# Kernel tuning notes

Hardware: AMD Instinct MI355X
Metric: run time of the kernel (lower is better)

Reference implementation:

```python
import jax, jax.numpy as jnp
import numpy as np

B, C, L = 4, 256, 2048
HEADS, DIM_HEAD = 8, 64
HIDDEN = HEADS * DIM_HEAD  # 512


def setup_inputs() -> dict:
    key = jax.random.key(0)
    k1, k2, k3, k4 = jax.random.split(key, 4)
    x = jax.random.normal(k1, (B, C, L), dtype=jnp.float32)
    # Conv1d kernel_size=1 weights, squeezed to [out_ch, in_ch]
    w_qkv = jax.random.normal(k2, (3 * HIDDEN, C), dtype=jnp.float32) * (1.0 / np.sqrt(C))
    w_out = jax.random.normal(k3, (C, HIDDEN), dtype=jnp.float32) * (1.0 / np.sqrt(HIDDEN))
    b_out = jax.random.normal(k4, (C,), dtype=jnp.float32) * 0.01
    return {"x": x, "w_qkv": w_qkv, "w_out": w_out, "b_out": b_out}


def reference(x, w_qkv, w_out, b_out):
    b, c, l = x.shape
    scale = DIM_HEAD ** (-0.5)
    # pointwise conv == channel matmul
    qkv = jnp.einsum('oc,bcl->bol', w_qkv, x)  # [b, 3*hidden, l]
    q, k, v = jnp.split(qkv, 3, axis=1)        # each [b, hidden, l]
    def to_heads(t):
        return t.reshape(b, HEADS, DIM_HEAD, l)  # b h d l
    q, k, v = to_heads(q), to_heads(k), to_heads(v)
    q = q * scale
    sim = jnp.einsum('bhdi,bhdj->bhij', q, k)   # [b,h,l,l]
    attn = jax.nn.softmax(sim, axis=-1)          # stable softmax (max-subtract inside)
    out = jnp.einsum('bhij,bhdj->bhid', attn, v)  # [b,h,l,d]
    out = out.transpose(0, 1, 3, 2).reshape(b, HIDDEN, l)  # b (h d) l
    return jnp.einsum('oc,bcl->bol', w_out, out) + b_out[None, :, None]
```

## Files before the change

### kernel.cpp

```cpp
#include <hip/hip_runtime.h>

typedef unsigned short u16;
typedef __bf16 bf16x8 __attribute__((ext_vector_type(8)));
typedef float f32x4 __attribute__((ext_vector_type(4)));

#define MFMA16(a, b, c) __builtin_amdgcn_mfma_f32_16x16x32_bf16((a), (b), (c), 0, 0, 0)

#define Bn 4
#define Cn 256
#define Ln 2048
#define Hn 8
#define Dn 64
#define HID 512

__device__ __forceinline__ u16 bf16_rne(float f) {
  unsigned u = __builtin_bit_cast(unsigned, f);
  u += 0x7FFFu + ((u >> 16) & 1u);
  return (u16)(u >> 16);
}

__device__ __forceinline__ unsigned pack2(float a, float b) {
  return (unsigned)bf16_rne(a) | ((unsigned)bf16_rne(b) << 16);
}

__device__ __forceinline__ float fast_exp2(float x) {
#if __has_builtin(__builtin_amdgcn_exp2f)
  return __builtin_amdgcn_exp2f(x);
#else
  return exp2f(x);
#endif
}

__device__ __forceinline__ float fast_rcp(float x) {
#if __has_builtin(__builtin_amdgcn_rcpf)
  return __builtin_amdgcn_rcpf(x);
#else
  return 1.0f / x;
#endif
}

__device__ __forceinline__ void async_load16(const u16* g, u16* l) {
  __builtin_amdgcn_global_load_lds(
      (const __attribute__((address_space(1))) void*)g,
      (__attribute__((address_space(3))) void*)l, 16, 0, 0);
}

__global__ __launch_bounds__(256) void prep_weights(const float* __restrict__ wqkv,
                                                    const float* __restrict__ wout,
                                                    u16* __restrict__ wq,
                                                    u16* __restrict__ wo) {
  int i = blockIdx.x * 256 + threadIdx.x;
  const float QSCALE = 0.125f * 1.44269504088896340736f;
  if (i < 3 * HID * Cn) {
    float v = wqkv[i];
    if (i < HID * Cn) v *= QSCALE;
    wq[i] = bf16_rne(v);
  } else {
    int j = i - 3 * HID * Cn;
    wo[j] = bf16_rne(wout[j]);
  }
}

__global__ __launch_bounds__(256) void transpose_x(const float* __restrict__ x,
                                                   u16* __restrict__ xT) {
  __shared__ u16 tile[64][72];
  const int b = blockIdx.z, ct = blockIdx.y, lt = blockIdx.x;
  const int t = threadIdx.x;
  const float* xp = x + ((size_t)b * Cn + ct * 64) * Ln + lt * 64;
  for (int pass = 0; pass < 4; ++pass) {
    int c = pass * 16 + (t >> 4);
    int l4 = (t & 15) * 4;
    float4 v = *(const float4*)(xp + (size_t)c * Ln + l4);
    tile[l4 + 0][c] = bf16_rne(v.x);
    tile[l4 + 1][c] = bf16_rne(v.y);
    tile[l4 + 2][c] = bf16_rne(v.z);
    tile[l4 + 3][c] = bf16_rne(v.w);
  }
  __syncthreads();
  u16* op = xT + ((size_t)b * Ln + lt * 64) * Cn + ct * 64;
  for (int pass = 0; pass < 2; ++pass) {
    int id = pass * 256 + t;
    int l = id >> 3, c8 = (id & 7) * 8;
    *(uint4*)(op + (size_t)l * Cn + c8) = *(const uint4*)&tile[l][c8];
  }
}

__global__ __launch_bounds__(256) void qkv_gemm(const u16* __restrict__ wq,
                                                const u16* __restrict__ xT,
                                                u16* __restrict__ qT,
                                                u16* __restrict__ kT,
                                                u16* __restrict__ vv) {
  __shared__ u16 As[4096];
  __shared__ u16 Bs[4096];
  const int t = threadIdx.x;
  const int nt = blockIdx.x, mt = blockIdx.y, b = blockIdx.z;
  const int m0 = mt * 64, n0 = nt * 64;
  const int w = t >> 6, lane = t & 63, q = lane >> 4, ln = lane & 15;

  const u16* Ag = wq + (size_t)m0 * Cn;
  const u16* Bg = xT + ((size_t)b * Ln + n0) * Cn;

  f32x4 zf = {0.f, 0.f, 0.f, 0.f};
  f32x4 acc[4];
  for (int i = 0; i < 4; ++i) acc[i] = zf;

  for (int kk = 0; kk < 4; ++kk) {
    int k0 = kk * 64;
    for (int k2 = 0; k2 < 2; ++k2) {
      int reg = k2 * 4 + w;
      int r = reg * 8 + (lane >> 3);
      int c = (lane & 7) ^ (r & 7);
      async_load16(Ag + (size_t)r * Cn + k0 + c * 8, &As[reg * 512]);
      async_load16(Bg + (size_t)r * Cn + k0 + c * 8, &Bs[reg * 512]);
    }
    __syncthreads();
    int ar = w * 16 + ln;
    bf16x8 a0 = *(const bf16x8*)&As[ar * 64 + ((q ^ (ln & 7)) * 8)];
    bf16x8 a1 = *(const bf16x8*)&As[ar * 64 + (((q + 4) ^ (ln & 7)) * 8)];
    for (int n2 = 0; n2 < 4; ++n2) {
      int br = n2 * 16 + ln;
      bf16x8 b0 = *(const bf16x8*)&Bs[br * 64 + ((q ^ (ln & 7)) * 8)];
      bf16x8 b1 = *(const bf16x8*)&Bs[br * 64 + (((q + 4) ^ (ln & 7)) * 8)];
      acc[n2] = MFMA16(a0, b0, acc[n2]);
      acc[n2] = MFMA16(a1, b1, acc[n2]);
    }
    __syncthreads();
  }

  if (mt < 16) {
    int od0 = w * 16 + q * 4;
    int cw = od0 >> 3, lo = od0 & 7;
    for (int n2 = 0; n2 < 4; ++n2) {
      int l = n2 * 16 + ln;
      uint2 pk;
      pk.x = pack2(acc[n2][0], acc[n2][1]);
      pk.y = pack2(acc[n2][2], acc[n2][3]);
      *(uint2*)&As[l * 64 + ((cw ^ (l & 7)) * 8) + lo] = pk;
    }
    __syncthreads();
    u16* dst = (mt < 8) ? qT + (((size_t)b * Hn + mt) * Ln + n0) * Dn
                        : kT + (((size_t)b * Hn + (mt - 8)) * Ln + n0) * Dn;
    for (int pass = 0; pass < 2; ++pass) {
      int id = pass * 256 + t;
      int l = id >> 3, c = id & 7;
      *(uint4*)(dst + (size_t)l * Dn + c * 8) =
          *(const uint4*)&As[l * 64 + ((c ^ (l & 7)) * 8)];
    }
  } else {
    for (int n2 = 0; n2 < 4; ++n2) {
      int l = n2 * 16 + ln;
      int cl = l >> 3, lo = l & 7;
      for (int r = 0; r < 4; ++r) {
        int od = w * 16 + q * 4 + r;
        As[od * 64 + ((cl ^ (od & 7)) * 8) + lo] = bf16_rne(acc[n2][r]);
      }
    }
    __syncthreads();
    u16* dst = vv + ((size_t)b * HID + (mt - 16) * 64) * Ln + n0;
    for (int pass = 0; pass < 2; ++pass) {
      int id = pass * 256 + t;
      int od = id >> 3, c = id & 7;
      *(uint4*)(dst + (size_t)od * Ln + c * 8) =
          *(const uint4*)&As[od * 64 + ((c ^ (od & 7)) * 8)];
    }
  }
}

__global__ __launch_bounds__(256) void attention(const u16* __restrict__ qT,
                                                 const u16* __restrict__ kT,
                                                 const u16* __restrict__ vv,
                                                 u16* __restrict__ attT) {
  __shared__ u16 Kt[4096];
  __shared__ u16 Vt[4096];
  __shared__ u16 Ps[8192];
  const int t = threadIdx.x;
  const int qb = blockIdx.x, bh = blockIdx.y;
  const int b = bh >> 3, h = bh & 7;
  const int w = t >> 6, lane = t & 63, q = lane >> 4, ln = lane & 15;
  const int i0 = qb * 128 + w * 32;

  bf16x8 qa00, qa01, qa10, qa11;
  {
    const u16* qrow0 = qT + (((size_t)bh) * Ln + i0 + ln) * Dn;
    const u16* qrow1 = qT + (((size_t)bh) * Ln + i0 + 16 + ln) * Dn;
    qa00 = *(const bf16x8*)(qrow0 + q * 8);
    qa01 = *(const bf16x8*)(qrow0 + 32 + q * 8);
    qa10 = *(const bf16x8*)(qrow1 + q * 8);
    qa11 = *(const bf16x8*)(qrow1 + 32 + q * 8);
  }

  const u16* ksrc0 = kT + ((size_t)bh) * Ln * Dn;
  const u16* vsrc0 = vv + ((size_t)b * HID + h * Dn) * Ln;

  bf16x8 ones;
  for (int i = 0; i < 8; ++i) ones[i] = (__bf16)1.0f;

  f32x4 zf = {0.f, 0.f, 0.f, 0.f};
  f32x4 o_acc[2][4], l_acc[2];
  for (int it = 0; it < 2; ++it) {
    l_acc[it] = zf;
    for (int d = 0; d < 4; ++d) o_acc[it][d] = zf;
  }
  u16* pw0 = Ps + w * 2048;

  const int pr0 = w * 8 + (lane >> 3), pr1 = (4 + w) * 8 + (lane >> 3);
  const int pc0 = (lane & 7) ^ (pr0 & 7), pc1 = (lane & 7) ^ (pr1 & 7);
  const u16* kadr0 = ksrc0 + (size_t)pr0 * Dn + pc0 * 8;
  const u16* kadr1 = ksrc0 + (size_t)pr1 * Dn + pc1 * 8;
  const u16* vadr0 = vsrc0 + (size_t)pr0 * Ln + pc0 * 8;
  const u16* vadr1 = vsrc0 + (size_t)pr1 * Ln + pc1 * 8;

#define LOADKV(jt, K0, K1, V0, V1)                              \
  {                                                             \
    int j0_ = (jt) * 64;                                        \
    K0 = *(const uint4*)(kadr0 + (size_t)j0_ * Dn);             \
    K1 = *(const uint4*)(kadr1 + (size_t)j0_ * Dn);             \
    V0 = *(const uint4*)(vadr0 + j0_);                          \
    V1 = *(const uint4*)(vadr1 + j0_);                          \
  }

#define STOREKV(K0, K1, V0, V1)                                 \
  {                                                             \
    *(uint4*)&Kt[w * 512 + lane * 8] = K0;                      \
    *(uint4*)&Kt[(4 + w) * 512 + lane * 8] = K1;                \
    *(uint4*)&Vt[w * 512 + lane * 8] = V0;                      \
    *(uint4*)&Vt[(4 + w) * 512 + lane * 8] = V1;                \
  }

#define COMPUTE()                                                              \
  {                                                                            \
    f32x4 sv[2][4];                                                            \
    for (int n2 = 0; n2 < 4; ++n2) {                                           \
      int jr = n2 * 16 + ln;                                                   \
      bf16x8 k0f = *(const bf16x8*)&Kt[jr * 64 + ((q ^ (ln & 7)) * 8)];        \
      bf16x8 k1f = *(const bf16x8*)&Kt[jr * 64 + (((q + 4) ^ (ln & 7)) * 8)];  \
      f32x4 s0 = zf, s1 = zf;                                                  \
      s0 = MFMA16(k0f, qa00, s0);                                              \
      s0 = MFMA16(k1f, qa01, s0);                                              \
      s1 = MFMA16(k0f, qa10, s1);                                              \
      s1 = MFMA16(k1f, qa11, s1);                                              \
      sv[0][n2] = s0;                                                          \
      sv[1][n2] = s1;                                                          \
    }                                                                          \
    for (int it = 0; it < 2; ++it) {                                           \
      u16* pw = pw0 + it * 1024;                                               \
      for (int n2 = 0; n2 < 4; ++n2) {                                         \
        uint2 pk;                                                              \
        pk.x = pack2(fast_exp2(sv[it][n2][0]), fast_exp2(sv[it][n2][1]));      \
        pk.y = pack2(fast_exp2(sv[it][n2][2]), fast_exp2(sv[it][n2][3]));      \
        int jw = n2 * 16 + q * 4;                                              \
        int c_ = jw >> 3, lo_ = jw & 7;                                        \
        *(uint2*)&pw[ln * 64 + ((c_ ^ (ln & 7)) * 8) + lo_] = pk;              \
      }                                                                        \
    }                                                                          \
    for (int it = 0; it < 2; ++it) {                                           \
      u16* pw = pw0 + it * 1024;                                               \
      bf16x8 pa0 = *(const bf16x8*)&pw[ln * 64 + ((q ^ (ln & 7)) * 8)];        \
      bf16x8 pa1 = *(const bf16x8*)&pw[ln * 64 + (((q + 4) ^ (ln & 7)) * 8)];  \
      l_acc[it] = MFMA16(pa0, ones, l_acc[it]);                                \
      l_acc[it] = MFMA16(pa1, ones, l_acc[it]);                                \
      for (int d2 = 0; d2 < 4; ++d2) {                                         \
        int dr = d2 * 16 + ln;                                                 \
        bf16x8 v0f = *(const bf16x8*)&Vt[dr * 64 + ((q ^ (ln & 7)) * 8)];      \
        bf16x8 v1f = *(const bf16x8*)&Vt[dr * 64 + (((q + 4) ^ (ln & 7)) * 8)];\
        o_acc[it][d2] = MFMA16(pa0, v0f, o_acc[it][d2]);                       \
        o_acc[it][d2] = MFMA16(pa1, v1f, o_acc[it][d2]);                       \
      }                                                                        \
    }                                                                          \
  }

  uint4 ka0, ka1, wa0, wa1, kb0, kb1, wb0, wb1;
  LOADKV(0, ka0, ka1, wa0, wa1);
  for (int jt = 0; jt < 32; jt += 2) {
    if (jt) __syncthreads();
    STOREKV(ka0, ka1, wa0, wa1);
    __syncthreads();
    LOADKV(jt + 1, kb0, kb1, wb0, wb1);
    COMPUTE();
    __syncthreads();
    STOREKV(kb0, kb1, wb0, wb1);
    __syncthreads();
    if (jt + 2 < 32) LOADKV(jt + 2, ka0, ka1, wa0, wa1);
    COMPUTE();
  }
#undef LOADKV
#undef STOREKV
#undef COMPUTE

  for (int it = 0; it < 2; ++it) {
    for (int r = 0; r < 4; ++r) {
      float rinv = fast_rcp(l_acc[it][r]);
      int i = i0 + it * 16 + q * 4 + r;
      size_t base = ((size_t)b * Ln + i) * HID + h * Dn;
      for (int d2 = 0; d2 < 4; ++d2)
        attT[base + d2 * 16 + ln] = bf16_rne(o_acc[it][d2][r] * rinv);
    }
  }
}

__global__ __launch_bounds__(256) void out_gemm(const u16* __restrict__ wo,
                                                const u16* __restrict__ attT,
                                                const float* __restrict__ bout,
                                                float* __restrict__ out) {
  __shared__ u16 As[4096];
  __shared__ u16 Bs[4096];
  const int t = threadIdx.x;
  const int nt = blockIdx.x, mt = blockIdx.y, b = blockIdx.z;
  const int m0 = mt * 64, n0 = nt * 64;
  const int w = t >> 6, lane = t & 63, q = lane >> 4, ln = lane & 15;

  const u16* Ag = wo + (size_t)m0 * HID;
  const u16* Bg = attT + ((size_t)b * Ln + n0) * HID;

  f32x4 zf = {0.f, 0.f, 0.f, 0.f};
  f32x4 acc[4];
  for (int i = 0; i < 4; ++i) acc[i] = zf;

  const int pr0 = w * 8 + (lane >> 3), pr1 = (4 + w) * 8 + (lane >> 3);
  const int pc0 = (lane & 7) ^ (pr0 & 7), pc1 = (lane & 7) ^ (pr1 & 7);
  const u16* Aad0 = Ag + (size_t)pr0 * HID + pc0 * 8;
  const u16* Aad1 = Ag + (size_t)pr1 * HID + pc1 * 8;
  const u16* Bad0 = Bg + (size_t)pr0 * HID + pc0 * 8;
  const u16* Bad1 = Bg + (size_t)pr1 * HID + pc1 * 8;

#define LOADAB(kk, A0, A1, B0, B1)               \
  {                                              \
    int k0_ = (kk) * 64;                         \
    A0 = *(const uint4*)(Aad0 + k0_);            \
    A1 = *(const uint4*)(Aad1 + k0_);            \
    B0 = *(const uint4*)(Bad0 + k0_);            \
    B1 = *(const uint4*)(Bad1 + k0_);            \
  }

#define STOREAB(A0, A1, B0, B1)                  \
  {                                              \
    *(uint4*)&As[w * 512 + lane * 8] = A0;       \
    *(uint4*)&As[(4 + w) * 512 + lane * 8] = A1; \
    *(uint4*)&Bs[w * 512 + lane * 8] = B0;       \
    *(uint4*)&Bs[(4 + w) * 512 + lane * 8] = B1; \
  }

#define COMPUTEC()                                                             \
  {                                                                            \
    int ar = w * 16 + ln;                                                      \
    bf16x8 a0 = *(const bf16x8*)&As[ar * 64 + ((q ^ (ln & 7)) * 8)];           \
    bf16x8 a1 = *(const bf16x8*)&As[ar * 64 + (((q + 4) ^ (ln & 7)) * 8)];     \
    for (int n2 = 0; n2 < 4; ++n2) {                                           \
      int br = n2 * 16 + ln;                                                   \
      bf16x8 b0 = *(const bf16x8*)&Bs[br * 64 + ((q ^ (ln & 7)) * 8)];         \
      bf16x8 b1 = *(const bf16x8*)&Bs[br * 64 + (((q + 4) ^ (ln & 7)) * 8)];   \
      acc[n2] = MFMA16(a0, b0, acc[n2]);                                       \
      acc[n2] = MFMA16(a1, b1, acc[n2]);                                       \
    }                                                                          \
  }

  uint4 aa0, aa1, ba0, ba1, ab0, ab1, bb0, bb1;
  LOADAB(0, aa0, aa1, ba0, ba1);
  for (int kk = 0; kk < 8; kk += 2) {
    if (kk) __syncthreads();
    STOREAB(aa0, aa1, ba0, ba1);
    __syncthreads();
    LOADAB(kk + 1, ab0, ab1, bb0, bb1);
    COMPUTEC();
    __syncthreads();
    STOREAB(ab0, ab1, bb0, bb1);
    __syncthreads();
    if (kk + 2 < 8) LOADAB(kk + 2, aa0, aa1, ba0, ba1);
    COMPUTEC();
  }
#undef LOADAB
#undef STOREAB
#undef COMPUTEC

  float bias[4];
  for (int r = 0; r < 4; ++r) bias[r] = bout[m0 + w * 16 + q * 4 + r];
  for (int n2 = 0; n2 < 4; ++n2) {
    int l = n0 + n2 * 16 + ln;
    for (int r = 0; r < 4; ++r) {
      int o = m0 + w * 16 + q * 4 + r;
      out[((size_t)b * Cn + o) * Ln + l] = acc[n2][r] + bias[r];
    }
  }
}

extern "C" void kernel_launch(void* const* d_in, const int* in_sizes, int n_in,
                              void* d_out, int out_size, void* d_ws, size_t ws_size,
                              hipStream_t stream) {
  const float* x = (const float*)d_in[0];
  const float* wqkv = (const float*)d_in[1];
  const float* wout = (const float*)d_in[2];
  const float* bout = (const float*)d_in[3];
  float* out = (float*)d_out;
  char* ws = (char*)d_ws;

  u16* wq_b = (u16*)(ws + 0);
  u16* wo_b = (u16*)(ws + 786432);
  u16* xT   = (u16*)(ws + 1048576);
  u16* qT   = (u16*)(ws + 5242880);
  u16* kT   = (u16*)(ws + 13631488);
  u16* vv   = (u16*)(ws + 22020096);
  u16* attT = (u16*)(ws + 30408704);

  prep_weights<<<2048, 256, 0, stream>>>(wqkv, wout, wq_b, wo_b);
  transpose_x<<<dim3(32, 4, 4), 256, 0, stream>>>(x, xT);
  qkv_gemm<<<dim3(32, 24, 4), 256, 0, stream>>>(wq_b, xT, qT, kT, vv);
  attention<<<dim3(16, 32), 256, 0, stream>>>(qT, kT, vv, attT);
  out_gemm<<<dim3(32, 4, 4), 256, 0, stream>>>(wo_b, attT, bout, out);
}
```

Baseline: 153.3 us.

## Switch attention to 32x32 MFMA, merge prep kernels, register-pipeline QKV GEMM

The attention kernel now uses 32x32x16 bf16 MFMA tiles. The row sum is accumulated in registers and combined with a lane shuffle, replacing the extra MFMA against a ones vector, and a cheaper round-to-nearest pack is used for P. The weight-prep and x-transpose kernels are merged into one launch to save a launch. The QKV GEMM replaces async global-to-LDS loads with a register double-buffered load/store pipeline. The main targets are MFMA instruction count and softmax overhead in the attention inner loop, at the cost of more registers per thread and a new output lane mapping.

```diff
diff --git a/kernel.cpp b/kernel.cpp
--- a/kernel.cpp
+++ b/kernel.cpp
@@ -1,10 +1,13 @@
 #include <hip/hip_runtime.h>
 
 typedef unsigned short u16;
+typedef unsigned int u32;
 typedef __bf16 bf16x8 __attribute__((ext_vector_type(8)));
 typedef float f32x4 __attribute__((ext_vector_type(4)));
+typedef float f32x16 __attribute__((ext_vector_type(16)));
 
 #define MFMA16(a, b, c) __builtin_amdgcn_mfma_f32_16x16x32_bf16((a), (b), (c), 0, 0, 0)
+#define MFMA32(a, b, c) __builtin_amdgcn_mfma_f32_32x32x16_bf16((a), (b), (c), 0, 0, 0)
 
 #define Bn 4
 #define Cn 256
@@ -14,13 +17,19 @@
 #define HID 512
 
 __device__ __forceinline__ u16 bf16_rne(float f) {
-  unsigned u = __builtin_bit_cast(unsigned, f);
+  u32 u = __builtin_bit_cast(u32, f);
   u += 0x7FFFu + ((u >> 16) & 1u);
   return (u16)(u >> 16);
 }
 
 __device__ __forceinline__ unsigned pack2(float a, float b) {
   return (unsigned)bf16_rne(a) | ((unsigned)bf16_rne(b) << 16);
+}
+
+__device__ __forceinline__ u32 pk_hi(float lo, float hi) {
+  u32 a = __builtin_bit_cast(u32, lo) + 0x8000u;
+  u32 b = __builtin_bit_cast(u32, hi) + 0x8000u;
+  return (b & 0xFFFF0000u) | (a >> 16);
 }
 
 __device__ __forceinline__ float fast_exp2(float x) {
@@ -39,42 +48,38 @@
 #endif
 }
 
-__device__ __forceinline__ void async_load16(const u16* g, u16* l) {
-  __builtin_amdgcn_global_load_lds(
-      (const __attribute__((address_space(1))) void*)g,
-      (__attribute__((address_space(3))) void*)l, 16, 0, 0);
-}
-
-__global__ __launch_bounds__(256) void prep_weights(const float* __restrict__ wqkv,
-                                                    const float* __restrict__ wout,
-                                                    u16* __restrict__ wq,
-                                                    u16* __restrict__ wo) {
-  int i = blockIdx.x * 256 + threadIdx.x;
-  const float QSCALE = 0.125f * 1.44269504088896340736f;
-  if (i < 3 * HID * Cn) {
-    float v = wqkv[i];
-    if (i < HID * Cn) v *= QSCALE;
-    wq[i] = bf16_rne(v);
-  } else {
-    int j = i - 3 * HID * Cn;
-    wo[j] = bf16_rne(wout[j]);
-  }
-}
-
-__global__ __launch_bounds__(256) void transpose_x(const float* __restrict__ x,
-                                                   u16* __restrict__ xT) {
+__global__ __launch_bounds__(256) void prep_all(const float* __restrict__ wqkv,
+                                                const float* __restrict__ wout,
+                                                const float* __restrict__ x,
+                                                u16* __restrict__ wq,
+                                                u16* __restrict__ wo,
+                                                u16* __restrict__ xT) {
+  const int t = threadIdx.x;
+  if (blockIdx.x < 2048) {
+    int i = blockIdx.x * 256 + t;
+    const float QSCALE = 0.125f * 1.44269504088896340736f;
+    if (i < 3 * HID * Cn) {
+      float v = wqkv[i];
+      if (i < HID * Cn) v *= QSCALE;
+      wq[i] = bf16_rne(v);
+    } else {
+      int j = i - 3 * HID * Cn;
+      wo[j] = bf16_rne(wout[j]);
+    }
+    return;
+  }
   __shared__ u16 tile[64][72];
-  const int b = blockIdx.z, ct = blockIdx.y, lt = blockIdx.x;
-  const int t = threadIdx.x;
+  int v = blockIdx.x - 2048;
+  const int lt = v & 31, ct = (v >> 5) & 3, b = v >> 7;
   const float* xp = x + ((size_t)b * Cn + ct * 64) * Ln + lt * 64;
   for (int pass = 0; pass < 4; ++pass) {
     int c = pass * 16 + (t >> 4);
     int l4 = (t & 15) * 4;
-    float4 v = *(const float4*)(xp + (size_t)c * Ln + l4);
-    tile[l4 + 0][c] = bf16_rne(v.x);
-    tile[l4 + 1][c] = bf16_rne(v.y);
-    tile[l4 + 2][c] = bf16_rne(v.z);
-    tile[l4 + 3][c] = bf16_rne(v.w);
+    float4 vf = *(const float4*)(xp + (size_t)c * Ln + l4);
+    tile[l4 + 0][c] = bf16_rne(vf.x);
+    tile[l4 + 1][c] = bf16_rne(vf.y);
+    tile[l4 + 2][c] = bf16_rne(vf.z);
+    tile[l4 + 3][c] = bf16_rne(vf.w);
   }
   __syncthreads();
   u16* op = xT + ((size_t)b * Ln + lt * 64) * Cn + ct * 64;
@@ -104,224 +109,12 @@
   f32x4 acc[4];
   for (int i = 0; i < 4; ++i) acc[i] = zf;
 
-  for (int kk = 0; kk < 4; ++kk) {
-    int k0 = kk * 64;
-    for (int k2 = 0; k2 < 2; ++k2) {
-      int reg = k2 * 4 + w;
-      int r = reg * 8 + (lane >> 3);
-      int c = (lane & 7) ^ (r & 7);
-      async_load16(Ag + (size_t)r * Cn + k0 + c * 8, &As[reg * 512]);
-      async_load16(Bg + (size_t)r * Cn + k0 + c * 8, &Bs[reg * 512]);
-    }
-    __syncthreads();
-    int ar = w * 16 + ln;
-    bf16x8 a0 = *(const bf16x8*)&As[ar * 64 + ((q ^ (ln & 7)) * 8)];
-    bf16x8 a1 = *(const bf16x8*)&As[ar * 64 + (((q + 4) ^ (ln & 7)) * 8)];
-    for (int n2 = 0; n2 < 4; ++n2) {
-      int br = n2 * 16 + ln;
-      bf16x8 b0 = *(const bf16x8*)&Bs[br * 64 + ((q ^ (ln & 7)) * 8)];
-      bf16x8 b1 = *(const bf16x8*)&Bs[br * 64 + (((q + 4) ^ (ln & 7)) * 8)];
-      acc[n2] = MFMA16(a0, b0, acc[n2]);
-      acc[n2] = MFMA16(a1, b1, acc[n2]);
-    }
-    __syncthreads();
-  }
-
-  if (mt < 16) {
-    int od0 = w * 16 + q * 4;
-    int cw = od0 >> 3, lo = od0 & 7;
-    for (int n2 = 0; n2 < 4; ++n2) {
-      int l = n2 * 16 + ln;
-      uint2 pk;
-      pk.x = pack2(acc[n2][0], acc[n2][1]);
-      pk.y = pack2(acc[n2][2], acc[n2][3]);
-      *(uint2*)&As[l * 64 + ((cw ^ (l & 7)) * 8) + lo] = pk;
-    }
-    __syncthreads();
-    u16* dst = (mt < 8) ? qT + (((size_t)b * Hn + mt) * Ln + n0) * Dn
-                        : kT + (((size_t)b * Hn + (mt - 8)) * Ln + n0) * Dn;
-    for (int pass = 0; pass < 2; ++pass) {
-      int id = pass * 256 + t;
-      int l = id >> 3, c = id & 7;
-      *(uint4*)(dst + (size_t)l * Dn + c * 8) =
-          *(const uint4*)&As[l * 64 + ((c ^ (l & 7)) * 8)];
-    }
-  } else {
-    for (int n2 = 0; n2 < 4; ++n2) {
-      int l = n2 * 16 + ln;
-      int cl = l >> 3, lo = l & 7;
-      for (int r = 0; r < 4; ++r) {
-        int od = w * 16 + q * 4 + r;
-        As[od * 64 + ((cl ^ (od & 7)) * 8) + lo] = bf16_rne(acc[n2][r]);
-      }
-    }
-    __syncthreads();
-    u16* dst = vv + ((size_t)b * HID + (mt - 16) * 64) * Ln + n0;
-    for (int pass = 0; pass < 2; ++pass) {
-      int id = pass * 256 + t;
-      int od = id >> 3, c = id & 7;
-      *(uint4*)(dst + (size_t)od * Ln + c * 8) =
-          *(const uint4*)&As[od * 64 + ((c ^ (od & 7)) * 8)];
-    }
-  }
-}
-
-__global__ __launch_bounds__(256) void attention(const u16* __restrict__ qT,
-                                                 const u16* __restrict__ kT,
-                                                 const u16* __restrict__ vv,
-                                                 u16* __restrict__ attT) {
-  __shared__ u16 Kt[4096];
-  __shared__ u16 Vt[4096];
-  __shared__ u16 Ps[8192];
-  const int t = threadIdx.x;
-  const int qb = blockIdx.x, bh = blockIdx.y;
-  const int b = bh >> 3, h = bh & 7;
-  const int w = t >> 6, lane = t & 63, q = lane >> 4, ln = lane & 15;
-  const int i0 = qb * 128 + w * 32;
-
-  bf16x8 qa00, qa01, qa10, qa11;
-  {
-    const u16* qrow0 = qT + (((size_t)bh) * Ln + i0 + ln) * Dn;
-    const u16* qrow1 = qT + (((size_t)bh) * Ln + i0 + 16 + ln) * Dn;
-    qa00 = *(const bf16x8*)(qrow0 + q * 8);
-    qa01 = *(const bf16x8*)(qrow0 + 32 + q * 8);
-    qa10 = *(const bf16x8*)(qrow1 + q * 8);
-    qa11 = *(const bf16x8*)(qrow1 + 32 + q * 8);
-  }
-
-  const u16* ksrc0 = kT + ((size_t)bh) * Ln * Dn;
-  const u16* vsrc0 = vv + ((size_t)b * HID + h * Dn) * Ln;
-
-  bf16x8 ones;
-  for (int i = 0; i < 8; ++i) ones[i] = (__bf16)1.0f;
-
-  f32x4 zf = {0.f, 0.f, 0.f, 0.f};
-  f32x4 o_acc[2][4], l_acc[2];
-  for (int it = 0; it < 2; ++it) {
-    l_acc[it] = zf;
-    for (int d = 0; d < 4; ++d) o_acc[it][d] = zf;
-  }
-  u16* pw0 = Ps + w * 2048;
-
   const int pr0 = w * 8 + (lane >> 3), pr1 = (4 + w) * 8 + (lane >> 3);
   const int pc0 = (lane & 7) ^ (pr0 & 7), pc1 = (lane & 7) ^ (pr1 & 7);
-  const u16* kadr0 = ksrc0 + (size_t)pr0 * Dn + pc0 * 8;
-  const u16* kadr1 = ksrc0 + (size_t)pr1 * Dn + pc1 * 8;
-  const u16* vadr0 = vsrc0 + (size_t)pr0 * Ln + pc0 * 8;
-  const u16* vadr1 = vsrc0 + (size_t)pr1 * Ln + pc1 * 8;
-
-#define LOADKV(jt, K0, K1, V0, V1)                              \
-  {                                                             \
-    int j0_ = (jt) * 64;                                        \
-    K0 = *(const uint4*)(kadr0 + (size_t)j0_ * Dn);             \
-    K1 = *(const uint4*)(kadr1 + (size_t)j0_ * Dn);             \
-    V0 = *(const uint4*)(vadr0 + j0_);                          \
-    V1 = *(const uint4*)(vadr1 + j0_);                          \
-  }
-
-#define STOREKV(K0, K1, V0, V1)                                 \
-  {                                                             \
-    *(uint4*)&Kt[w * 512 + lane * 8] = K0;                      \
-    *(uint4*)&Kt[(4 + w) * 512 + lane * 8] = K1;                \
-    *(uint4*)&Vt[w * 512 + lane * 8] = V0;                      \
-    *(uint4*)&Vt[(4 + w) * 512 + lane * 8] = V1;                \
-  }
-
-#define COMPUTE()                                                              \
-  {                                                                            \
-    f32x4 sv[2][4];                                                            \
-    for (int n2 = 0; n2 < 4; ++n2) {                                           \
-      int jr = n2 * 16 + ln;                                                   \
-      bf16x8 k0f = *(const bf16x8*)&Kt[jr * 64 + ((q ^ (ln & 7)) * 8)];        \
-      bf16x8 k1f = *(const bf16x8*)&Kt[jr * 64 + (((q + 4) ^ (ln & 7)) * 8)];  \
-      f32x4 s0 = zf, s1 = zf;                                                  \
-      s0 = MFMA16(k0f, qa00, s0);                                              \
-      s0 = MFMA16(k1f, qa01, s0);                                              \
-      s1 = MFMA16(k0f, qa10, s1);                                              \
-      s1 = MFMA16(k1f, qa11, s1);                                              \
-      sv[0][n2] = s0;                                                          \
-      sv[1][n2] = s1;                                                          \
-    }                                                                          \
-    for (int it = 0; it < 2; ++it) {                                           \
-      u16* pw = pw0 + it * 1024;                                               \
-      for (int n2 = 0; n2 < 4; ++n2) {                                         \
-        uint2 pk;                                                              \
-        pk.x = pack2(fast_exp2(sv[it][n2][0]), fast_exp2(sv[it][n2][1]));      \
-        pk.y = pack2(fast_exp2(sv[it][n2][2]), fast_exp2(sv[it][n2][3]));      \
-        int jw = n2 * 16 + q * 4;                                              \
-        int c_ = jw >> 3, lo_ = jw & 7;                                        \
-        *(uint2*)&pw[ln * 64 + ((c_ ^ (ln & 7)) * 8) + lo_] = pk;              \
-      }                                                                        \
-    }                                                                          \
-    for (int it = 0; it < 2; ++it) {                                           \
-      u16* pw = pw0 + it * 1024;                                               \
-      bf16x8 pa0 = *(const bf16x8*)&pw[ln * 64 + ((q ^ (ln & 7)) * 8)];        \
-      bf16x8 pa1 = *(const bf16x8*)&pw[ln * 64 + (((q + 4) ^ (ln & 7)) * 8)];  \
-      l_acc[it] = MFMA16(pa0, ones, l_acc[it]);                                \
-      l_acc[it] = MFMA16(pa1, ones, l_acc[it]);                                \
-      for (int d2 = 0; d2 < 4; ++d2) {                                         \
-        int dr = d2 * 16 + ln;                                                 \
-        bf16x8 v0f = *(const bf16x8*)&Vt[dr * 64 + ((q ^ (ln & 7)) * 8)];      \
-        bf16x8 v1f = *(const bf16x8*)&Vt[dr * 64 + (((q + 4) ^ (ln & 7)) * 8)];\
-        o_acc[it][d2] = MFMA16(pa0, v0f, o_acc[it][d2]);                       \
-        o_acc[it][d2] = MFMA16(pa1, v1f, o_acc[it][d2]);                       \
-      }                                                                        \
-    }                                                                          \
-  }
-
-  uint4 ka0, ka1, wa0, wa1, kb0, kb1, wb0, wb1;
-  LOADKV(0, ka0, ka1, wa0, wa1);
-  for (int jt = 0; jt < 32; jt += 2) {
-    if (jt) __syncthreads();
-    STOREKV(ka0, ka1, wa0, wa1);
-    __syncthreads();
-    LOADKV(jt + 1, kb0, kb1, wb0, wb1);
-    COMPUTE();
-    __syncthreads();
-    STOREKV(kb0, kb1, wb0, wb1);
-    __syncthreads();
-    if (jt + 2 < 32) LOADKV(jt + 2, ka0, ka1, wa0, wa1);
-    COMPUTE();
-  }
-#undef LOADKV
-#undef STOREKV
-#undef COMPUTE
-
-  for (int it = 0; it < 2; ++it) {
-    for (int r = 0; r < 4; ++r) {
-      float rinv = fast_rcp(l_acc[it][r]);
-      int i = i0 + it * 16 + q * 4 + r;
-      size_t base = ((size_t)b * Ln + i) * HID + h * Dn;
-      for (int d2 = 0; d2 < 4; ++d2)
-        attT[base + d2 * 16 + ln] = bf16_rne(o_acc[it][d2][r] * rinv);
-    }
-  }
-}
-
-__global__ __launch_bounds__(256) void out_gemm(const u16* __restrict__ wo,
-                                                const u16* __restrict__ attT,
-                                                const float* __restrict__ bout,
-                                                float* __restrict__ out) {
-  __shared__ u16 As[4096];
-  __shared__ u16 Bs[4096];
-  const int t = threadIdx.x;
-  const int nt = blockIdx.x, mt = blockIdx.y, b = blockIdx.z;
-  const int m0 = mt * 64, n0 = nt * 64;
-  const int w = t >> 6, lane = t & 63, q = lane >> 4, ln = lane & 15;
-
-  const u16* Ag = wo + (size_t)m0 * HID;
-  const u16* Bg = attT + ((size_t)b * Ln + n0) * HID;
-
-  f32x4 zf = {0.f, 0.f, 0.f, 0.f};
-  f32x4 acc[4];
-  for (int i = 0; i < 4; ++i) acc[i] = zf;
-
-  const int pr0 = w * 8 + (lane >> 3), pr1 = (4 + w) * 8 + (lane >> 3);
-  const int pc0 = (lane & 7) ^ (pr0 & 7), pc1 = (lane & 7) ^ (pr1 & 7);
-  const u16* Aad0 = Ag + (size_t)pr0 * HID + pc0 * 8;
-  const u16* Aad1 = Ag + (size_t)pr1 * HID + pc1 * 8;
-  const u16* Bad0 = Bg + (size_t)pr0 * HID + pc0 * 8;
-  const u16* Bad1 = Bg + (size_t)pr1 * HID + pc1 * 8;
+  const u16* Aad0 = Ag + (size_t)pr0 * Cn + pc0 * 8;
+  const u16* Aad1 = Ag + (size_t)pr1 * Cn + pc1 * 8;
+  const u16* Bad0 = Bg + (size_t)pr0 * Cn + pc0 * 8;
+  const u16* Bad1 = Bg + (size_t)pr1 * Cn + pc1 * 8;
 
 #define LOADAB(kk, A0, A1, B0, B1)               \
   {                                              \
@@ -331,7 +124,6 @@
     B0 = *(const uint4*)(Bad0 + k0_);            \
     B1 = *(const uint4*)(Bad1 + k0_);            \
   }
-
 #define STOREAB(A0, A1, B0, B1)                  \
   {                                              \
     *(uint4*)&As[w * 512 + lane * 8] = A0;       \
@@ -339,7 +131,6 @@
     *(uint4*)&Bs[w * 512 + lane * 8] = B0;       \
     *(uint4*)&Bs[(4 + w) * 512 + lane * 8] = B1; \
   }
-
 #define COMPUTEC()                                                             \
   {                                                                            \
     int ar = w * 16 + ln;                                                      \
@@ -356,6 +147,243 @@
 
   uint4 aa0, aa1, ba0, ba1, ab0, ab1, bb0, bb1;
   LOADAB(0, aa0, aa1, ba0, ba1);
+  for (int kk = 0; kk < 4; kk += 2) {
+    if (kk) __syncthreads();
+    STOREAB(aa0, aa1, ba0, ba1);
+    __syncthreads();
+    LOADAB(kk + 1, ab0, ab1, bb0, bb1);
+    COMPUTEC();
+    __syncthreads();
+    STOREAB(ab0, ab1, bb0, bb1);
+    __syncthreads();
+    if (kk + 2 < 4) LOADAB(kk + 2, aa0, aa1, ba0, ba1);
+    COMPUTEC();
+  }
+#undef LOADAB
+#undef STOREAB
+#undef COMPUTEC
+
+  __syncthreads();
+  if (mt < 16) {
+    int od0 = w * 16 + q * 4;
+    int cw = od0 >> 3, lo = od0 & 7;
+    for (int n2 = 0; n2 < 4; ++n2) {
+      int l = n2 * 16 + ln;
+      uint2 pk;
+      pk.x = pack2(acc[n2][0], acc[n2][1]);
+      pk.y = pack2(acc[n2][2], acc[n2][3]);
+      *(uint2*)&As[l * 64 + ((cw ^ (l & 7)) * 8) + lo] = pk;
+    }
+    __syncthreads();
+    u16* dst = (mt < 8) ? qT + (((size_t)b * Hn + mt) * Ln + n0) * Dn
+                        : kT + (((size_t)b * Hn + (mt - 8)) * Ln + n0) * Dn;
+    for (int pass = 0; pass < 2; ++pass) {
+      int id = pass * 256 + t;
+      int l = id >> 3, c = id & 7;
+      *(uint4*)(dst + (size_t)l * Dn + c * 8) =
+          *(const uint4*)&As[l * 64 + ((c ^ (l & 7)) * 8)];
+    }
+  } else {
+    for (int n2 = 0; n2 < 4; ++n2) {
+      int l = n2 * 16 + ln;
+      int cl = l >> 3, lo = l & 7;
+      for (int r = 0; r < 4; ++r) {
+        int od = w * 16 + q * 4 + r;
+        As[od * 64 + ((cl ^ (od & 7)) * 8) + lo] = bf16_rne(acc[n2][r]);
+      }
+    }
+    __syncthreads();
+    u16* dst = vv + ((size_t)b * HID + (mt - 16) * 64) * Ln + n0;
+    for (int pass = 0; pass < 2; ++pass) {
+      int id = pass * 256 + t;
+      int od = id >> 3, c = id & 7;
+      *(uint4*)(dst + (size_t)od * Ln + c * 8) =
+          *(const uint4*)&As[od * 64 + ((c ^ (od & 7)) * 8)];
+    }
+  }
+}
+
+__global__ __launch_bounds__(256) void attention(const u16* __restrict__ qT,
+                                                 const u16* __restrict__ kT,
+                                                 const u16* __restrict__ vv,
+                                                 u16* __restrict__ attT) {
+  __shared__ u16 Kt[4096];
+  __shared__ u16 Vt[4096];
+  __shared__ u16 Ps[8192];
+  const int t = threadIdx.x;
+  const int qb = blockIdx.x, bh = blockIdx.y;
+  const int b = bh >> 3, hh = bh & 7;
+  const int w = t >> 6, lane = t & 63;
+  const int li = lane & 31, h = lane >> 5;
+  const int i0 = qb * 128 + w * 32;
+
+  bf16x8 qf0, qf1, qf2, qf3;
+  {
+    const u16* qrow = qT + (((size_t)bh) * Ln + i0 + li) * Dn + h * 8;
+    qf0 = *(const bf16x8*)(qrow + 0);
+    qf1 = *(const bf16x8*)(qrow + 16);
+    qf2 = *(const bf16x8*)(qrow + 32);
+    qf3 = *(const bf16x8*)(qrow + 48);
+  }
+
+  const u16* ksrc0 = kT + ((size_t)bh) * Ln * Dn;
+  const u16* vsrc0 = vv + ((size_t)b * HID + hh * Dn) * Ln;
+
+  f32x16 o0, o1;
+#pragma unroll
+  for (int r = 0; r < 16; ++r) { o0[r] = 0.f; o1[r] = 0.f; }
+  float lp = 0.f;
+  u16* pw = Ps + w * 2048;
+
+  const int pr0 = w * 8 + (lane >> 3), pr1 = (4 + w) * 8 + (lane >> 3);
+  const int pc0 = (lane & 7) ^ (pr0 & 7), pc1 = (lane & 7) ^ (pr1 & 7);
+  const u16* kadr0 = ksrc0 + (size_t)pr0 * Dn + pc0 * 8;
+  const u16* kadr1 = ksrc0 + (size_t)pr1 * Dn + pc1 * 8;
+  const u16* vadr0 = vsrc0 + (size_t)pr0 * Ln + pc0 * 8;
+  const u16* vadr1 = vsrc0 + (size_t)pr1 * Ln + pc1 * 8;
+
+#define LOADKV(jt, K0, K1, V0, V1)                              \
+  {                                                             \
+    int j0_ = (jt) * 64;                                        \
+    K0 = *(const uint4*)(kadr0 + (size_t)j0_ * Dn);             \
+    K1 = *(const uint4*)(kadr1 + (size_t)j0_ * Dn);             \
+    V0 = *(const uint4*)(vadr0 + j0_);                          \
+    V1 = *(const uint4*)(vadr1 + j0_);                          \
+  }
+#define STOREKV(K0, K1, V0, V1)                                 \
+  {                                                             \
+    *(uint4*)&Kt[w * 512 + lane * 8] = K0;                      \
+    *(uint4*)&Kt[(4 + w) * 512 + lane * 8] = K1;                \
+    *(uint4*)&Vt[w * 512 + lane * 8] = V0;                      \
+    *(uint4*)&Vt[(4 + w) * 512 + lane * 8] = V1;                \
+  }
+
+#define COMPUTE()                                                              \
+  {                                                                            \
+    f32x16 sv0, sv1;                                                           \
+    _Pragma("unroll") for (int r = 0; r < 16; ++r) { sv0[r] = 0.f; sv1[r] = 0.f; } \
+    _Pragma("unroll") for (int c = 0; c < 4; ++c) {                            \
+      int ch = 2 * c + h;                                                      \
+      bf16x8 k0 = *(const bf16x8*)&Kt[li * 64 + ((ch ^ (li & 7)) * 8)];        \
+      bf16x8 k1 = *(const bf16x8*)&Kt[(32 + li) * 64 + ((ch ^ (li & 7)) * 8)]; \
+      bf16x8 qc = (c == 0) ? qf0 : (c == 1) ? qf1 : (c == 2) ? qf2 : qf3;      \
+      sv0 = MFMA32(k0, qc, sv0);                                               \
+      sv1 = MFMA32(k1, qc, sv1);                                               \
+    }                                                                          \
+    _Pragma("unroll") for (int js = 0; js < 2; ++js) {                         \
+      _Pragma("unroll") for (int g = 0; g < 4; ++g) {                          \
+        float e0 = fast_exp2(js ? sv1[4 * g + 0] : sv0[4 * g + 0]);            \
+        float e1 = fast_exp2(js ? sv1[4 * g + 1] : sv0[4 * g + 1]);            \
+        float e2 = fast_exp2(js ? sv1[4 * g + 2] : sv0[4 * g + 2]);            \
+        float e3 = fast_exp2(js ? sv1[4 * g + 3] : sv0[4 * g + 3]);            \
+        lp += (e0 + e1) + (e2 + e3);                                           \
+        uint2 pk;                                                              \
+        pk.x = pk_hi(e0, e1);                                                  \
+        pk.y = pk_hi(e2, e3);                                                  \
+        int cjj = js * 4 + g;                                                  \
+        *(uint2*)&pw[li * 64 + ((cjj ^ (li & 7)) * 8) + 4 * h] = pk;           \
+      }                                                                        \
+    }                                                                          \
+    bf16x8 pf0 = *(const bf16x8*)&pw[li * 64 + (((2 * 0 + h) ^ (li & 7)) * 8)];\
+    bf16x8 pf1 = *(const bf16x8*)&pw[li * 64 + (((2 * 1 + h) ^ (li & 7)) * 8)];\
+    bf16x8 pf2 = *(const bf16x8*)&pw[li * 64 + (((2 * 2 + h) ^ (li & 7)) * 8)];\
+    bf16x8 pf3 = *(const bf16x8*)&pw[li * 64 + (((2 * 3 + h) ^ (li & 7)) * 8)];\
+    _Pragma("unroll") for (int jc = 0; jc < 4; ++jc) {                         \
+      int ch = 2 * jc + h;                                                     \
+      bf16x8 pf = (jc == 0) ? pf0 : (jc == 1) ? pf1 : (jc == 2) ? pf2 : pf3;   \
+      bf16x8 vf0 = *(const bf16x8*)&Vt[li * 64 + ((ch ^ (li & 7)) * 8)];       \
+      bf16x8 vf1 = *(const bf16x8*)&Vt[(32 + li) * 64 + ((ch ^ (li & 7)) * 8)];\
+      o0 = MFMA32(pf, vf0, o0);                                                \
+      o1 = MFMA32(pf, vf1, o1);                                                \
+    }                                                                          \
+  }
+
+  uint4 ka0, ka1, wa0, wa1, kb0, kb1, wb0, wb1;
+  LOADKV(0, ka0, ka1, wa0, wa1);
+  for (int jt = 0; jt < 32; jt += 2) {
+    if (jt) __syncthreads();
+    STOREKV(ka0, ka1, wa0, wa1);
+    __syncthreads();
+    LOADKV(jt + 1, kb0, kb1, wb0, wb1);
+    COMPUTE();
+    __syncthreads();
+    STOREKV(kb0, kb1, wb0, wb1);
+    __syncthreads();
+    if (jt + 2 < 32) LOADKV(jt + 2, ka0, ka1, wa0, wa1);
+    COMPUTE();
+  }
+#undef LOADKV
+#undef STOREKV
+#undef COMPUTE
+
+  float lsum = lp + __shfl_xor(lp, 32);
+  float linv = fast_rcp(lsum);
+#pragma unroll
+  for (int r = 0; r < 16; ++r) {
+    int ir = (r & 3) + 8 * (r >> 2) + 4 * h;
+    float lv = __shfl(linv, ir);
+    size_t base = ((size_t)b * Ln + i0 + ir) * HID + hh * Dn + li;
+    attT[base] = bf16_rne(o0[r] * lv);
+    attT[base + 32] = bf16_rne(o1[r] * lv);
+  }
+}
+
+__global__ __launch_bounds__(256) void out_gemm(const u16* __restrict__ wo,
+                                                const u16* __restrict__ attT,
+                                                const float* __restrict__ bout,
+                                                float* __restrict__ out) {
+  __shared__ u16 As[4096];
+  __shared__ u16 Bs[4096];
+  const int t = threadIdx.x;
+  const int nt = blockIdx.x, mt = blockIdx.y, b = blockIdx.z;
+  const int m0 = mt * 64, n0 = nt * 64;
+  const int w = t >> 6, lane = t & 63, q = lane >> 4, ln = lane & 15;
+
+  const u16* Ag = wo + (size_t)m0 * HID;
+  const u16* Bg = attT + ((size_t)b * Ln + n0) * HID;
+
+  f32x4 zf = {0.f, 0.f, 0.f, 0.f};
+  f32x4 acc[4];
+  for (int i = 0; i < 4; ++i) acc[i] = zf;
+
+  const int pr0 = w * 8 + (lane >> 3), pr1 = (4 + w) * 8 + (lane >> 3);
+  const int pc0 = (lane & 7) ^ (pr0 & 7), pc1 = (lane & 7) ^ (pr1 & 7);
+  const u16* Aad0 = Ag + (size_t)pr0 * HID + pc0 * 8;
+  const u16* Aad1 = Ag + (size_t)pr1 * HID + pc1 * 8;
+  const u16* Bad0 = Bg + (size_t)pr0 * HID + pc0 * 8;
+  const u16* Bad1 = Bg + (size_t)pr1 * HID + pc1 * 8;
+
+#define LOADAB(kk, A0, A1, B0, B1)               \
+  {                                              \
+    int k0_ = (kk) * 64;                         \
+    A0 = *(const uint4*)(Aad0 + k0_);            \
+    A1 = *(const uint4*)(Aad1 + k0_);            \
+    B0 = *(const uint4*)(Bad0 + k0_);            \
+    B1 = *(const uint4*)(Bad1 + k0_);            \
+  }
+#define STOREAB(A0, A1, B0, B1)                  \
+  {                                              \
+    *(uint4*)&As[w * 512 + lane * 8] = A0;       \
+    *(uint4*)&As[(4 + w) * 512 + lane * 8] = A1; \
+    *(uint4*)&Bs[w * 512 + lane * 8] = B0;       \
+    *(uint4*)&Bs[(4 + w) * 512 + lane * 8] = B1; \
+  }
+#define COMPUTEC()                                                             \
+  {                                                                            \
+    int ar = w * 16 + ln;                                                      \
+    bf16x8 a0 = *(const bf16x8*)&As[ar * 64 + ((q ^ (ln & 7)) * 8)];           \
+    bf16x8 a1 = *(const bf16x8*)&As[ar * 64 + (((q + 4) ^ (ln & 7)) * 8)];     \
+    for (int n2 = 0; n2 < 4; ++n2) {                                           \
+      int br = n2 * 16 + ln;                                                   \
+      bf16x8 b0 = *(const bf16x8*)&Bs[br * 64 + ((q ^ (ln & 7)) * 8)];         \
+      bf16x8 b1 = *(const bf16x8*)&Bs[br * 64 + (((q + 4) ^ (ln & 7)) * 8)];   \
+      acc[n2] = MFMA16(a0, b0, acc[n2]);                                       \
+      acc[n2] = MFMA16(a1, b1, acc[n2]);                                       \
+    }                                                                          \
+  }
+
+  uint4 aa0, aa1, ba0, ba1, ab0, ab1, bb0, bb1;
+  LOADAB(0, aa0, aa1, ba0, ba1);
   for (int kk = 0; kk < 8; kk += 2) {
     if (kk) __syncthreads();
     STOREAB(aa0, aa1, ba0, ba1);
@@ -401,8 +429,7 @@
   u16* vv   = (u16*)(ws + 22020096);
   u16* attT = (u16*)(ws + 30408704);
 
-  prep_weights<<<2048, 256, 0, stream>>>(wqkv, wout, wq_b, wo_b);
-  transpose_x<<<dim3(32, 4, 4), 256, 0, stream>>>(x, xT);
+  prep_all<<<2560, 256, 0, stream>>>(wqkv, wout, x, wq_b, wo_b, xT);
   qkv_gemm<<<dim3(32, 24, 4), 256, 0, stream>>>(wq_b, xT, qT, kT, vv);
   attention<<<dim3(16, 32), 256, 0, stream>>>(qT, kT, vv, attT);
   out_gemm<<<dim3(32, 4, 4), 256, 0, stream>>>(wo_b, attT, bout, out);
```

Measured after the change: 142.6 us. 1.08x faster.
